# Kernel tuning notes

Hardware: AMD Instinct MI355X
Metric: run time of the kernel (lower is better)

The kernel has to match this reference:

```python
import jax, jax.numpy as jnp
import numpy as np

HEAD_SIZE = 32


def setup_inputs() -> dict:
    key = jax.random.key(0)
    ks = jax.random.split(key, 9)
    B, N, M = 2, 512, 512
    Dq = Dk = Dv = 128
    De = 64
    H, O, OUT = 8, HEAD_SIZE, 128
    s = 0.05  # keep logits tame
    return {
        "query": jax.random.normal(ks[0], (B, N, Dq), jnp.float32),
        "key": jax.random.normal(ks[1], (B, M, Dk), jnp.float32),
        "value": jax.random.normal(ks[2], (B, M, Dv), jnp.float32),
        "edge": jax.random.normal(ks[3], (B, N, M, De), jnp.float32),
        "query_kernel": jax.random.normal(ks[4], (H, Dq, O), jnp.float32) * s,
        "key_kernel": jax.random.normal(ks[5], (H, Dk + De, O), jnp.float32) * s,
        "value_kernel": jax.random.normal(ks[6], (H, Dv, O), jnp.float32) * s,
        "projection_kernel": jax.random.normal(ks[7], (H, O, OUT), jnp.float32) * s,
        "projection_bias": jnp.zeros((OUT,), jnp.float32),
    }


def reference(query, key, value, edge, query_kernel, key_kernel,
              value_kernel, projection_kernel, projection_bias):
    # Edge-conditioned keys: concat broadcast key [B,1,M,Dk] with edge [B,N,M,De]
    B, N, _ = query.shape
    M = key.shape[-2]
    key_rep = jnp.broadcast_to(key[..., None, :, :], (B, N, M, key.shape[-1]))
    key_cat = jnp.concatenate([key_rep, edge], axis=-1)           # [B,N,M,Dk+De]
    k = jnp.einsum('bnmi,hio->bnmho', key_cat, key_kernel)        # [B,N,M,H,O]
    q = jnp.einsum('bni,hio->bnho', query, query_kernel)
    q = q / jnp.sqrt(jnp.asarray(HEAD_SIZE, q.dtype))
    v = jnp.einsum('bmi,hio->bmho', value, value_kernel)
    logits = jnp.einsum('bnho,bnmho->bhnm', q, k)                 # [B,H,N,M]
    attn = jax.nn.softmax(logits, axis=-1)
    mh = jnp.einsum('bhnm,bmho->bnho', attn, v)                   # [B,N,H,O]
    out = jnp.einsum('bnhi,hio->bno', mh, projection_kernel)
    out = out + projection_bias
    return out
```

## Files before the change

### kernel.cpp

```cpp
#include <hip/hip_runtime.h>
#include <hip/hip_bf16.h>

#define B_   2
#define N_   512
#define M_   512
#define D_   128
#define DE_  64
#define H_   8
#define O_   32
#define OUT_ 128
#define DKE_ 192
#define MP_  516

typedef unsigned short u16;
typedef unsigned int   u32;
typedef short bf16x8 __attribute__((ext_vector_type(8)));
typedef float floatx4 __attribute__((ext_vector_type(4)));

__device__ __forceinline__ u32 pk2bf(float a, float b) {
    __hip_bfloat162 h = __float22bfloat162_rn(make_float2(a, b));
    return *reinterpret_cast<u32*>(&h);
}
__device__ __forceinline__ u16 f2bf(float a) {
    __hip_bfloat16 h = __float2bfloat16(a);
    return *reinterpret_cast<u16*>(&h);
}
__device__ __forceinline__ bf16x8 cvt8(const float4 a, const float4 b) {
    union { u32 u[4]; bf16x8 v; } r;
    r.u[0] = pk2bf(a.x, a.y); r.u[1] = pk2bf(a.z, a.w);
    r.u[2] = pk2bf(b.x, b.y); r.u[3] = pk2bf(b.z, b.w);
    return r.v;
}

__global__ __launch_bounds__(256) void k_proj(
    const float* __restrict__ query, const float* __restrict__ Wq,
    const float* __restrict__ Wk,
    const float* __restrict__ value, const float* __restrict__ Wv,
    const float* __restrict__ key,
    u16* __restrict__ qE, u16* __restrict__ vP, u16* __restrict__ keyF)
{
    const int t = threadIdx.x;
    __shared__ float Xs[8][D_];
    __shared__ float qh[8][H_ * O_];

    if (blockIdx.x < 128) {
        const int r0 = blockIdx.x * 8;
        reinterpret_cast<float4*>(&Xs[0][0])[t] =
            reinterpret_cast<const float4*>(query + (size_t)r0 * D_)[t];
        __syncthreads();
        {
            float acc[8] = {0,0,0,0,0,0,0,0};
            const float* wcol = Wq + (t >> 5) * (D_ * O_) + (t & 31);
            for (int k = 0; k < D_; k += 4) {
                const float w0 = wcol[(k+0) * O_];
                const float w1 = wcol[(k+1) * O_];
                const float w2 = wcol[(k+2) * O_];
                const float w3 = wcol[(k+3) * O_];
#pragma unroll
                for (int r = 0; r < 8; ++r) {
                    const float4 x = *reinterpret_cast<const float4*>(&Xs[r][k]);
                    acc[r] += x.x * w0 + x.y * w1 + x.z * w2 + x.w * w3;
                }
            }
#pragma unroll
            for (int r = 0; r < 8; ++r) qh[r][t] = acc[r] * 0.17677669529663687f;
        }
        __syncthreads();

        for (int s = 0; s < 6; ++s) {
            const int hj = t + 256 * s;
            const int h  = hj / DKE_;
            float w[O_];
#pragma unroll
            for (int i = 0; i < O_ / 4; ++i) {
                const float4 x = reinterpret_cast<const float4*>(Wk + (size_t)hj * O_)[i];
                w[4*i] = x.x; w[4*i+1] = x.y; w[4*i+2] = x.z; w[4*i+3] = x.w;
            }
#pragma unroll
            for (int r = 0; r < 8; ++r) {
                const float* qrow = &qh[r][h * O_];
                float a = 0.f;
#pragma unroll
                for (int i = 0; i < O_ / 4; ++i) {
                    const float4 qx = *reinterpret_cast<const float4*>(qrow + 4*i);
                    a += qx.x * w[4*i] + qx.y * w[4*i+1] + qx.z * w[4*i+2] + qx.w * w[4*i+3];
                }
                qE[(size_t)(r0 + r) * (H_ * DKE_) + hj] = f2bf(a);
            }
        }
    } else if (blockIdx.x < 256) {
        const int r0 = (blockIdx.x - 128) * 8;
        reinterpret_cast<float4*>(&Xs[0][0])[t] =
            reinterpret_cast<const float4*>(value + (size_t)r0 * D_)[t];
        __syncthreads();

        float acc[8] = {0,0,0,0,0,0,0,0};
        const float* wcol = Wv + (t >> 5) * (D_ * O_) + (t & 31);
        for (int k = 0; k < D_; k += 4) {
            const float w0 = wcol[(k+0) * O_];
            const float w1 = wcol[(k+1) * O_];
            const float w2 = wcol[(k+2) * O_];
            const float w3 = wcol[(k+3) * O_];
#pragma unroll
            for (int r = 0; r < 8; ++r) {
                const float4 x = *reinterpret_cast<const float4*>(&Xs[r][k]);
                acc[r] += x.x * w0 + x.y * w1 + x.z * w2 + x.w * w3;
            }
        }
        const int bb = r0 >> 9, m0 = r0 & 511;
        union { u32 u[4]; uint4 q; } pk;
        pk.u[0] = pk2bf(acc[0], acc[1]);
        pk.u[1] = pk2bf(acc[2], acc[3]);
        pk.u[2] = pk2bf(acc[4], acc[5]);
        pk.u[3] = pk2bf(acc[6], acc[7]);
        *reinterpret_cast<uint4*>(
            vP + ((((size_t)bb * 64) + (m0 >> 3)) * 256 + t) * 8) = pk.q;
    } else {
        const int kb = blockIdx.x - 256;
        const int bb = kb >> 5, tl = kb & 31;
        const int kk = t >> 6, l = t & 63;
        const int br = l & 15, q = l >> 4;
        const float* src = key + ((size_t)bb * M_ + tl * 16 + br) * D_ + kk * 32 + q * 8;
        const float4 f0 = *reinterpret_cast<const float4*>(src);
        const float4 f1 = *reinterpret_cast<const float4*>(src + 4);
        union { bf16x8 v; uint4 u; } r;
        r.v = cvt8(f0, f1);
        *reinterpret_cast<uint4*>(
            keyF + ((((size_t)bb * 32 + tl) * 4 + kk) * 64 + l) * 8) = r.u;
    }
}

__global__ __launch_bounds__(512, 8) void k_attn(
    const float* __restrict__ edge,
    const u16* __restrict__ qE, const u16* __restrict__ vP,
    const u16* __restrict__ keyF,
    const float* __restrict__ Wp, const float* __restrict__ bias,
    float* __restrict__ out)
{
    const int idx  = blockIdx.x;
    const int b    = idx >> 9;
    const int t    = threadIdx.x;
    const int lane = t & 63;
    const int wv   = t >> 6;

    __shared__ __attribute__((aligned(16))) float attn_s[H_][MP_];
    __shared__ __attribute__((aligned(16))) u16 elds[8][1024];
    __shared__ float mh_s[2][256];
    __shared__ float part_s[4][OUT_];

    const int br = lane & 15;
    const int q  = lane >> 4;

    const int base16 = ((lane >> 1) & 15) * 16 + ((lane >> 5) << 1) + (lane & 1);

    const float4* tb = reinterpret_cast<const float4*>(edge + (size_t)idx * (M_ * DE_));
    float4 ef[4];
#pragma unroll
    for (int i = 0; i < 4; ++i)
        ef[i] = tb[wv * 256 + base16 + i * 4];

    bf16x8 afr[6];
    if (br < 8) {
        const u16* ab = qE + (size_t)idx * (H_ * DKE_) + br * DKE_;
#pragma unroll
        for (int kk = 0; kk < 6; ++kk)
            afr[kk] = *reinterpret_cast<const bf16x8*>(ab + kk * 32 + q * 8);
    } else {
#pragma unroll
        for (int kk = 0; kk < 6; ++kk) afr[kk] = bf16x8{0,0,0,0,0,0,0,0};
    }

    const u16* kfb = keyF + (size_t)b * (32 * 4 * 64 * 8);

    for (int it = 0; it < 4; ++it) {
        const int tl = it * 8 + wv;
#pragma unroll
        for (int i = 0; i < 4; ++i) {
            uint2 p;
            p.x = pk2bf(ef[i].x, ef[i].y); p.y = pk2bf(ef[i].z, ef[i].w);
            *reinterpret_cast<uint2*>(&elds[wv][i * 256 + lane * 4]) = p;
        }
        if (it < 3) {
#pragma unroll
            for (int i = 0; i < 4; ++i)
                ef[i] = tb[(tl + 8) * 256 + base16 + i * 4];
        }
        floatx4 acc = {0.f, 0.f, 0.f, 0.f};
        const u16* kf = kfb + (size_t)tl * 2048 + lane * 8;
#pragma unroll
        for (int kk = 0; kk < 4; ++kk) {
            const bf16x8 bfr = *reinterpret_cast<const bf16x8*>(kf + kk * 512);
            acc = __builtin_amdgcn_mfma_f32_16x16x32_bf16(afr[kk], bfr, acc, 0, 0, 0);
        }
#pragma unroll
        for (int kk = 0; kk < 2; ++kk) {
            const bf16x8 bfr = *reinterpret_cast<const bf16x8*>(&elds[wv][(kk * 64 + lane) * 8]);
            acc = __builtin_amdgcn_mfma_f32_16x16x32_bf16(afr[4 + kk], bfr, acc, 0, 0, 0);
        }
        if (q < 2) {
#pragma unroll
            for (int i = 0; i < 4; ++i)
                attn_s[q * 4 + i][tl * 16 + br] = acc[i];
        }
    }
    __syncthreads();

    {
        const int h = wv, ml = lane;
        float mx = -3.4e38f;
#pragma unroll
        for (int j = 0; j < 8; ++j) mx = fmaxf(mx, attn_s[h][ml + 64 * j]);
#pragma unroll
        for (int mask = 32; mask >= 1; mask >>= 1) mx = fmaxf(mx, __shfl_xor(mx, mask, 64));
        float sum = 0.f;
#pragma unroll
        for (int j = 0; j < 8; ++j) {
            const int m = ml + 64 * j;
            const float p = __expf(attn_s[h][m] - mx);
            attn_s[h][m] = p;
            sum += p;
        }
#pragma unroll
        for (int mask = 32; mask >= 1; mask >>= 1) sum += __shfl_xor(sum, mask, 64);
        const float inv = 1.f / sum;
#pragma unroll
        for (int j = 0; j < 8; ++j) attn_s[h][ml + 64 * j] *= inv;
    }
    __syncthreads();

    {
        const int tt = t & 255, half = t >> 8, hh = tt >> 5;
        const u16* vb = vP + (size_t)b * (64 * 256 * 8)
                      + ((size_t)(half * 32) * 256 + tt) * 8;
        const int mbase = half * 256;
        float a0 = 0.f, a1 = 0.f;
#pragma unroll 8
        for (int j = 0; j < 32; ++j) {
            const uint4 v4 = *reinterpret_cast<const uint4*>(vb + (size_t)j * 2048);
            const int m0 = mbase + j * 8;
            const float4 w0 = *reinterpret_cast<const float4*>(&attn_s[hh][m0]);
            const float4 w1 = *reinterpret_cast<const float4*>(&attn_s[hh][m0 + 4]);
            const float v0 = __uint_as_float(v4.x << 16);
            const float v1 = __uint_as_float(v4.x & 0xffff0000u);
            const float v2 = __uint_as_float(v4.y << 16);
            const float v3 = __uint_as_float(v4.y & 0xffff0000u);
            const float v4f = __uint_as_float(v4.z << 16);
            const float v5 = __uint_as_float(v4.z & 0xffff0000u);
            const float v6 = __uint_as_float(v4.w << 16);
            const float v7 = __uint_as_float(v4.w & 0xffff0000u);
            a0 += w0.x * v0 + w0.y * v1 + w0.z * v2 + w0.w * v3;
            a1 += w1.x * v4f + w1.y * v5 + w1.z * v6 + w1.w * v7;
        }
        mh_s[half][tt] = a0 + a1;
    }
    __syncthreads();

    {
        const int seg = t >> 7, c = t & 127;
        const int j0 = seg * 64;
        float acc = 0.f;
#pragma unroll 8
        for (int jj = 0; jj < 64; ++jj) {
            const int j = j0 + jj;
            acc += (mh_s[0][j] + mh_s[1][j]) * Wp[(size_t)j * OUT_ + c];
        }
        part_s[seg][c] = acc;
    }
    __syncthreads();
    if (t < OUT_)
        out[(size_t)idx * OUT_ + t] = part_s[0][t] + part_s[1][t]
                                    + part_s[2][t] + part_s[3][t] + bias[t];
}

extern "C" void kernel_launch(void* const* d_in, const int* in_sizes, int n_in,
                              void* d_out, int out_size, void* d_ws, size_t ws_size,
                              hipStream_t stream)
{
    const float* query = (const float*)d_in[0];
    const float* key   = (const float*)d_in[1];
    const float* value = (const float*)d_in[2];
    const float* edge  = (const float*)d_in[3];
    const float* Wq    = (const float*)d_in[4];
    const float* Wk    = (const float*)d_in[5];
    const float* Wv    = (const float*)d_in[6];
    const float* Wp    = (const float*)d_in[7];
    const float* bias  = (const float*)d_in[8];
    float* out = (float*)d_out;

    u16* qE_ws = (u16*)d_ws;
    u16* vP_ws = qE_ws + (size_t)B_ * N_ * H_ * DKE_;
    u16* kF_ws = vP_ws + (size_t)B_ * 64 * 256 * 8;

    k_proj<<<320,  256, 0, stream>>>(query, Wq, Wk, value, Wv, key, qE_ws, vP_ws, kF_ws);
    k_attn<<<1024, 512, 0, stream>>>(edge, qE_ws, vP_ws, kF_ws, Wp, bias, out);
}
```

Measured before the change: 241.9 us.

## Split attention into logits/softmax kernel and separate PV-projection kernel

The fused attention kernel is split in two. The first computes logits and softmax and writes the fp32 attention probabilities to a global workspace. A new 256-thread kernel reloads them, does the P·V reduction and the output projection. This aims to shorten the edge-streaming kernel and lower its register and LDS pressure so occupancy rises. In exchange it adds roughly 16 MB of global write plus read traffic and an extra launch. The key-fragment loads are also hoisted ahead of the edge conversion.

```diff
diff --git a/kernel.cpp b/kernel.cpp
--- a/kernel.cpp
+++ b/kernel.cpp
@@ -132,10 +132,8 @@
 
 __global__ __launch_bounds__(512, 8) void k_attn(
     const float* __restrict__ edge,
-    const u16* __restrict__ qE, const u16* __restrict__ vP,
-    const u16* __restrict__ keyF,
-    const float* __restrict__ Wp, const float* __restrict__ bias,
-    float* __restrict__ out)
+    const u16* __restrict__ qE, const u16* __restrict__ keyF,
+    float* __restrict__ attnP)
 {
     const int idx  = blockIdx.x;
     const int b    = idx >> 9;
@@ -145,8 +143,6 @@
 
     __shared__ __attribute__((aligned(16))) float attn_s[H_][MP_];
     __shared__ __attribute__((aligned(16))) u16 elds[8][1024];
-    __shared__ float mh_s[2][256];
-    __shared__ float part_s[4][OUT_];
 
     const int br = lane & 15;
     const int q  = lane >> 4;
@@ -174,6 +170,11 @@
 
     for (int it = 0; it < 4; ++it) {
         const int tl = it * 8 + wv;
+        const u16* kf = kfb + (size_t)tl * 2048 + lane * 8;
+        bf16x8 bk0 = *reinterpret_cast<const bf16x8*>(kf);
+        bf16x8 bk1 = *reinterpret_cast<const bf16x8*>(kf + 512);
+        bf16x8 bk2 = *reinterpret_cast<const bf16x8*>(kf + 1024);
+        bf16x8 bk3 = *reinterpret_cast<const bf16x8*>(kf + 1536);
 #pragma unroll
         for (int i = 0; i < 4; ++i) {
             uint2 p;
@@ -186,12 +187,10 @@
                 ef[i] = tb[(tl + 8) * 256 + base16 + i * 4];
         }
         floatx4 acc = {0.f, 0.f, 0.f, 0.f};
-        const u16* kf = kfb + (size_t)tl * 2048 + lane * 8;
-#pragma unroll
-        for (int kk = 0; kk < 4; ++kk) {
-            const bf16x8 bfr = *reinterpret_cast<const bf16x8*>(kf + kk * 512);
-            acc = __builtin_amdgcn_mfma_f32_16x16x32_bf16(afr[kk], bfr, acc, 0, 0, 0);
-        }
+        acc = __builtin_amdgcn_mfma_f32_16x16x32_bf16(afr[0], bk0, acc, 0, 0, 0);
+        acc = __builtin_amdgcn_mfma_f32_16x16x32_bf16(afr[1], bk1, acc, 0, 0, 0);
+        acc = __builtin_amdgcn_mfma_f32_16x16x32_bf16(afr[2], bk2, acc, 0, 0, 0);
+        acc = __builtin_amdgcn_mfma_f32_16x16x32_bf16(afr[3], bk3, acc, 0, 0, 0);
 #pragma unroll
         for (int kk = 0; kk < 2; ++kk) {
             const bf16x8 bfr = *reinterpret_cast<const bf16x8*>(&elds[wv][(kk * 64 + lane) * 8]);
@@ -229,17 +228,45 @@
     __syncthreads();
 
     {
-        const int tt = t & 255, half = t >> 8, hh = tt >> 5;
-        const u16* vb = vP + (size_t)b * (64 * 256 * 8)
-                      + ((size_t)(half * 32) * 256 + tt) * 8;
-        const int mbase = half * 256;
+        const int h = t >> 6, m0 = (t & 63) * 8;
+        float* dst = attnP + ((size_t)idx * H_ + h) * M_ + m0;
+        *reinterpret_cast<float4*>(dst)     = *reinterpret_cast<const float4*>(&attn_s[h][m0]);
+        *reinterpret_cast<float4*>(dst + 4) = *reinterpret_cast<const float4*>(&attn_s[h][m0 + 4]);
+    }
+}
+
+__global__ __launch_bounds__(256, 8) void k_pv(
+    const float* __restrict__ attnP, const u16* __restrict__ vP,
+    const float* __restrict__ Wp, const float* __restrict__ bias,
+    float* __restrict__ out)
+{
+    const int idx = blockIdx.x;
+    const int b   = idx >> 9;
+    const int t   = threadIdx.x;
+
+    __shared__ __attribute__((aligned(16))) float attn_ld[H_ * M_];
+    __shared__ float mh_s[256];
+    __shared__ float part_s[2][OUT_];
+
+    {
+        const float4* src = reinterpret_cast<const float4*>(attnP + (size_t)idx * (H_ * M_));
+        float4* dst = reinterpret_cast<float4*>(attn_ld);
+#pragma unroll
+        for (int i = 0; i < 4; ++i)
+            dst[i * 256 + t] = src[i * 256 + t];
+    }
+    __syncthreads();
+
+    {
+        const int hh = t >> 5;
+        const float* wrow = attn_ld + hh * M_;
+        const u16* vb = vP + (size_t)b * (64 * 256 * 8) + (size_t)t * 8;
         float a0 = 0.f, a1 = 0.f;
 #pragma unroll 8
-        for (int j = 0; j < 32; ++j) {
+        for (int j = 0; j < 64; ++j) {
             const uint4 v4 = *reinterpret_cast<const uint4*>(vb + (size_t)j * 2048);
-            const int m0 = mbase + j * 8;
-            const float4 w0 = *reinterpret_cast<const float4*>(&attn_s[hh][m0]);
-            const float4 w1 = *reinterpret_cast<const float4*>(&attn_s[hh][m0 + 4]);
+            const float4 w0 = *reinterpret_cast<const float4*>(wrow + j * 8);
+            const float4 w1 = *reinterpret_cast<const float4*>(wrow + j * 8 + 4);
             const float v0 = __uint_as_float(v4.x << 16);
             const float v1 = __uint_as_float(v4.x & 0xffff0000u);
             const float v2 = __uint_as_float(v4.y << 16);
@@ -251,25 +278,23 @@
             a0 += w0.x * v0 + w0.y * v1 + w0.z * v2 + w0.w * v3;
             a1 += w1.x * v4f + w1.y * v5 + w1.z * v6 + w1.w * v7;
         }
-        mh_s[half][tt] = a0 + a1;
-    }
-    __syncthreads();
-
-    {
-        const int seg = t >> 7, c = t & 127;
-        const int j0 = seg * 64;
+        mh_s[t] = a0 + a1;
+    }
+    __syncthreads();
+
+    {
+        const int half = t >> 7;
+        const int c = t & 127;
         float acc = 0.f;
+        const int j0 = half * 128;
 #pragma unroll 8
-        for (int jj = 0; jj < 64; ++jj) {
-            const int j = j0 + jj;
-            acc += (mh_s[0][j] + mh_s[1][j]) * Wp[(size_t)j * OUT_ + c];
-        }
-        part_s[seg][c] = acc;
+        for (int jj = 0; jj < 128; ++jj)
+            acc += mh_s[j0 + jj] * Wp[(size_t)(j0 + jj) * OUT_ + c];
+        part_s[half][c] = acc;
     }
     __syncthreads();
     if (t < OUT_)
-        out[(size_t)idx * OUT_ + t] = part_s[0][t] + part_s[1][t]
-                                    + part_s[2][t] + part_s[3][t] + bias[t];
+        out[(size_t)idx * OUT_ + t] = part_s[0][t] + part_s[1][t] + bias[t];
 }
 
 extern "C" void kernel_launch(void* const* d_in, const int* in_sizes, int n_in,
@@ -287,10 +312,12 @@
     const float* bias  = (const float*)d_in[8];
     float* out = (float*)d_out;
 
-    u16* qE_ws = (u16*)d_ws;
+    float* attnP = (float*)d_ws;
+    u16* qE_ws = (u16*)((char*)d_ws + (size_t)B_*N_*H_*M_*4);
     u16* vP_ws = qE_ws + (size_t)B_ * N_ * H_ * DKE_;
     u16* kF_ws = vP_ws + (size_t)B_ * 64 * 256 * 8;
 
     k_proj<<<320,  256, 0, stream>>>(query, Wq, Wk, value, Wv, key, qE_ws, vP_ws, kF_ws);
-    k_attn<<<1024, 512, 0, stream>>>(edge, qE_ws, vP_ws, kF_ws, Wp, bias, out);
-}
+    k_attn<<<1024, 512, 0, stream>>>(edge, qE_ws, kF_ws, attnP);
+    k_pv  <<<1024, 256, 0, stream>>>(attnP, vP_ws, Wp, bias, out);
+}
```

Result: slower. 262.3 us (+8.4%).

## Precompute key-part logits in separate kernel via projected keys

Applied to the files above, without the earlier changes.

Splits the logits into a key term and an edge term. Keys are projected per head in k_proj, and a new k_qk kernel computes q·k_h logits with MFMA into a float32 workspace. k_attn then loads those partial logits instead of running the key MFMAs, and only does the edge contraction. This removes per-block key MFMAs and keyF loads, but adds a 16MB logits write and read plus an extra kernel launch.

```diff
diff --git a/kernel.cpp b/kernel.cpp
--- a/kernel.cpp
+++ b/kernel.cpp
@@ -25,19 +25,14 @@
     __hip_bfloat16 h = __float2bfloat16(a);
     return *reinterpret_cast<u16*>(&h);
 }
-__device__ __forceinline__ bf16x8 cvt8(const float4 a, const float4 b) {
-    union { u32 u[4]; bf16x8 v; } r;
-    r.u[0] = pk2bf(a.x, a.y); r.u[1] = pk2bf(a.z, a.w);
-    r.u[2] = pk2bf(b.x, b.y); r.u[3] = pk2bf(b.z, b.w);
-    return r.v;
-}
 
 __global__ __launch_bounds__(256) void k_proj(
     const float* __restrict__ query, const float* __restrict__ Wq,
     const float* __restrict__ Wk,
     const float* __restrict__ value, const float* __restrict__ Wv,
     const float* __restrict__ key,
-    u16* __restrict__ qE, u16* __restrict__ vP, u16* __restrict__ keyF)
+    u16* __restrict__ qh_ws, u16* __restrict__ qE_e,
+    u16* __restrict__ vP, u16* __restrict__ khb)
 {
     const int t = threadIdx.x;
     __shared__ float Xs[8][D_];
@@ -63,17 +58,23 @@
                 }
             }
 #pragma unroll
-            for (int r = 0; r < 8; ++r) qh[r][t] = acc[r] * 0.17677669529663687f;
+            for (int r = 0; r < 8; ++r) {
+                const float v = acc[r] * 0.17677669529663687f;
+                qh[r][t] = v;
+                qh_ws[(size_t)(r0 + r) * 256 + t] = f2bf(v);
+            }
         }
         __syncthreads();
 
-        for (int s = 0; s < 6; ++s) {
+#pragma unroll
+        for (int s = 0; s < 2; ++s) {
             const int hj = t + 256 * s;
-            const int h  = hj / DKE_;
+            const int h  = hj >> 6, j = hj & 63;
             float w[O_];
 #pragma unroll
             for (int i = 0; i < O_ / 4; ++i) {
-                const float4 x = reinterpret_cast<const float4*>(Wk + (size_t)hj * O_)[i];
+                const float4 x = reinterpret_cast<const float4*>(
+                    Wk + (size_t)(h * DKE_ + 128 + j) * O_)[i];
                 w[4*i] = x.x; w[4*i+1] = x.y; w[4*i+2] = x.z; w[4*i+3] = x.w;
             }
 #pragma unroll
@@ -85,7 +86,7 @@
                     const float4 qx = *reinterpret_cast<const float4*>(qrow + 4*i);
                     a += qx.x * w[4*i] + qx.y * w[4*i+1] + qx.z * w[4*i+2] + qx.w * w[4*i+3];
                 }
-                qE[(size_t)(r0 + r) * (H_ * DKE_) + hj] = f2bf(a);
+                qE_e[(size_t)(r0 + r) * 512 + hj] = f2bf(a);
             }
         }
     } else if (blockIdx.x < 256) {
@@ -116,24 +117,65 @@
         *reinterpret_cast<uint4*>(
             vP + ((((size_t)bb * 64) + (m0 >> 3)) * 256 + t) * 8) = pk.q;
     } else {
-        const int kb = blockIdx.x - 256;
-        const int bb = kb >> 5, tl = kb & 31;
-        const int kk = t >> 6, l = t & 63;
-        const int br = l & 15, q = l >> 4;
-        const float* src = key + ((size_t)bb * M_ + tl * 16 + br) * D_ + kk * 32 + q * 8;
-        const float4 f0 = *reinterpret_cast<const float4*>(src);
-        const float4 f1 = *reinterpret_cast<const float4*>(src + 4);
-        union { bf16x8 v; uint4 u; } r;
-        r.v = cvt8(f0, f1);
-        *reinterpret_cast<uint4*>(
-            keyF + ((((size_t)bb * 32 + tl) * 4 + kk) * 64 + l) * 8) = r.u;
+        const int r0 = (blockIdx.x - 256) * 8;
+        reinterpret_cast<float4*>(&Xs[0][0])[t] =
+            reinterpret_cast<const float4*>(key + (size_t)r0 * D_)[t];
+        __syncthreads();
+
+        float acc[8] = {0,0,0,0,0,0,0,0};
+        const int h = t >> 5, o = t & 31;
+        const float* wcol = Wk + (size_t)h * (DKE_ * O_) + o;
+        for (int k = 0; k < D_; k += 4) {
+            const float w0 = wcol[(k+0) * O_];
+            const float w1 = wcol[(k+1) * O_];
+            const float w2 = wcol[(k+2) * O_];
+            const float w3 = wcol[(k+3) * O_];
+#pragma unroll
+            for (int r = 0; r < 8; ++r) {
+                const float4 x = *reinterpret_cast<const float4*>(&Xs[r][k]);
+                acc[r] += x.x * w0 + x.y * w1 + x.z * w2 + x.w * w3;
+            }
+        }
+        const int bb = r0 >> 9, m0 = r0 & 511;
+        u16* dst = khb + (((size_t)(bb * 8 + h) * 512) + m0) * 32 + o;
+#pragma unroll
+        for (int r = 0; r < 8; ++r) dst[(size_t)r * 32] = f2bf(acc[r]);
+    }
+}
+
+__global__ __launch_bounds__(256, 8) void k_qk(
+    const u16* __restrict__ qh_ws, const u16* __restrict__ khb,
+    float* __restrict__ qkL)
+{
+    const int bid = blockIdx.x;
+    const int b  = bid >> 8, h = (bid >> 5) & 7, nc = (bid >> 2) & 7, mc = bid & 3;
+    const int t = threadIdx.x;
+    const int lane = t & 63, wv = t >> 6;
+    const int br = lane & 15, q = lane >> 4;
+
+    const int ntl = nc * 4 + wv;
+    const bf16x8 afr = *reinterpret_cast<const bf16x8*>(
+        qh_ws + ((size_t)(b * 512 + ntl * 16 + br)) * 256 + h * 32 + q * 8);
+    const u16* kb = khb + ((size_t)(b * 8 + h) * 512) * 32;
+
+#pragma unroll
+    for (int mt = 0; mt < 8; ++mt) {
+        const int mtl = mc * 8 + mt;
+        const bf16x8 bfr = *reinterpret_cast<const bf16x8*>(
+            kb + (size_t)(mtl * 16 + br) * 32 + q * 8);
+        floatx4 z = {0.f, 0.f, 0.f, 0.f};
+        const floatx4 acc = __builtin_amdgcn_mfma_f32_16x16x32_bf16(afr, bfr, z, 0, 0, 0);
+        float* base = qkL + (size_t)(b * 512 + ntl * 16 + q * 4) * 4096
+                    + mtl * 128 + (h >> 2) * 64 + (h & 3) * 16 + br;
+#pragma unroll
+        for (int i = 0; i < 4; ++i) base[(size_t)i * 4096] = acc[i];
     }
 }
 
 __global__ __launch_bounds__(512, 8) void k_attn(
     const float* __restrict__ edge,
-    const u16* __restrict__ qE, const u16* __restrict__ vP,
-    const u16* __restrict__ keyF,
+    const u16* __restrict__ qE_e, const float* __restrict__ qkL,
+    const u16* __restrict__ vP,
     const float* __restrict__ Wp, const float* __restrict__ bias,
     float* __restrict__ out)
 {
@@ -159,21 +201,29 @@
     for (int i = 0; i < 4; ++i)
         ef[i] = tb[wv * 256 + base16 + i * 4];
 
-    bf16x8 afr[6];
+    bf16x8 afr[2];
     if (br < 8) {
-        const u16* ab = qE + (size_t)idx * (H_ * DKE_) + br * DKE_;
-#pragma unroll
-        for (int kk = 0; kk < 6; ++kk)
+        const u16* ab = qE_e + (size_t)idx * 512 + br * 64;
+#pragma unroll
+        for (int kk = 0; kk < 2; ++kk)
             afr[kk] = *reinterpret_cast<const bf16x8*>(ab + kk * 32 + q * 8);
     } else {
 #pragma unroll
-        for (int kk = 0; kk < 6; ++kk) afr[kk] = bf16x8{0,0,0,0,0,0,0,0};
-    }
-
-    const u16* kfb = keyF + (size_t)b * (32 * 4 * 64 * 8);
+        for (int kk = 0; kk < 2; ++kk) afr[kk] = bf16x8{0,0,0,0,0,0,0,0};
+    }
+
+    const float* qb = qkL + (size_t)idx * 4096;
 
     for (int it = 0; it < 4; ++it) {
         const int tl = it * 8 + wv;
+        floatx4 acc;
+        if (q < 2) {
+            const float* qt = qb + tl * 128 + q * 64 + br;
+#pragma unroll
+            for (int i = 0; i < 4; ++i) acc[i] = qt[i * 16];
+        } else {
+            acc = floatx4{0.f, 0.f, 0.f, 0.f};
+        }
 #pragma unroll
         for (int i = 0; i < 4; ++i) {
             uint2 p;
@@ -185,17 +235,10 @@
             for (int i = 0; i < 4; ++i)
                 ef[i] = tb[(tl + 8) * 256 + base16 + i * 4];
         }
-        floatx4 acc = {0.f, 0.f, 0.f, 0.f};
-        const u16* kf = kfb + (size_t)tl * 2048 + lane * 8;
-#pragma unroll
-        for (int kk = 0; kk < 4; ++kk) {
-            const bf16x8 bfr = *reinterpret_cast<const bf16x8*>(kf + kk * 512);
-            acc = __builtin_amdgcn_mfma_f32_16x16x32_bf16(afr[kk], bfr, acc, 0, 0, 0);
-        }
 #pragma unroll
         for (int kk = 0; kk < 2; ++kk) {
             const bf16x8 bfr = *reinterpret_cast<const bf16x8*>(&elds[wv][(kk * 64 + lane) * 8]);
-            acc = __builtin_amdgcn_mfma_f32_16x16x32_bf16(afr[4 + kk], bfr, acc, 0, 0, 0);
+            acc = __builtin_amdgcn_mfma_f32_16x16x32_bf16(afr[kk], bfr, acc, 0, 0, 0);
         }
         if (q < 2) {
 #pragma unroll
@@ -287,10 +330,14 @@
     const float* bias  = (const float*)d_in[8];
     float* out = (float*)d_out;
 
-    u16* qE_ws = (u16*)d_ws;
-    u16* vP_ws = qE_ws + (size_t)B_ * N_ * H_ * DKE_;
-    u16* kF_ws = vP_ws + (size_t)B_ * 64 * 256 * 8;
-
-    k_proj<<<320,  256, 0, stream>>>(query, Wq, Wk, value, Wv, key, qE_ws, vP_ws, kF_ws);
-    k_attn<<<1024, 512, 0, stream>>>(edge, qE_ws, vP_ws, kF_ws, Wp, bias, out);
-}
+    float* qkL  = (float*)d_ws;
+    u16* qh_ws  = (u16*)((char*)d_ws + (size_t)16 * 1024 * 1024);
+    u16* qEe_ws = qh_ws + (size_t)1024 * 256;
+    u16* vP_ws  = qEe_ws + (size_t)1024 * 512;
+    u16* khb_ws = vP_ws + (size_t)B_ * 64 * 256 * 8;
+
+    k_proj<<<384,  256, 0, stream>>>(query, Wq, Wk, value, Wv, key,
+                                     qh_ws, qEe_ws, vP_ws, khb_ws);
+    k_qk  <<<512,  256, 0, stream>>>(qh_ws, khb_ws, qkL);
+    k_attn<<<1024, 512, 0, stream>>>(edge, qEe_ws, qkL, vP_ws, Wp, bias, out);
+}
```

New measurement: 242.0 us. No clear change (+0.0%).
